# Kernel tuning notes

Measured on AMD Instinct MI355X. Metric: run time of the kernel, lower is better.

The kernel has to match this reference:

```python
import jax, jax.numpy as jnp
import numpy as np

H = 8
D_MODEL = 512
D_K = D_MODEL // H
B = 8
S = 1024


def _linear(x, W, b):
    # torch nn.Linear: y = x @ W.T + b, W: [out, in]
    return jnp.einsum('bsd,ed->bse', x, W) + b


def _to_heads(x):
    # [B,S,D] -> [B,H,S,d_k]
    return x.reshape(B, S, H, D_K).transpose(0, 2, 1, 3)


def setup_inputs() -> dict:
    key = jax.random.key(0)
    ks = jax.random.split(key, 20)
    inp = {
        'input_rgb': jax.random.normal(ks[0], (B, S, D_MODEL), jnp.float32),
        'input_flow': jax.random.normal(ks[1], (B, S, D_MODEL), jnp.float32),
    }
    names = ['Wq1', 'Wk1', 'Wv1', 'Wq2', 'Wk2', 'Wv2', 'Wo1', 'Wo2']
    for i, n in enumerate(names):
        inp[n] = jax.random.normal(ks[2 + i], (D_MODEL, D_MODEL), jnp.float32) * 0.02
        inp['b' + n[1:]] = jax.random.normal(ks[10 + i], (D_MODEL,), jnp.float32) * 0.02
    return inp


def reference(input_rgb, input_flow, Wq1, bq1, Wk1, bk1, Wv1, bv1,
              Wq2, bq2, Wk2, bk2, Wv2, bv2, Wo1, bo1, Wo2, bo2):
    scale = 1.0 / jnp.sqrt(jnp.asarray(D_K, input_rgb.dtype))

    q_r = _to_heads(_linear(input_rgb, Wq1, bq1))
    k_r = _to_heads(_linear(input_rgb, Wk1, bk1))
    v_r = _to_heads(_linear(input_rgb, Wv1, bv1))
    q_f = _to_heads(_linear(input_flow, Wq2, bq2))
    k_f = _to_heads(_linear(input_flow, Wk2, bk2))
    v_f = _to_heads(_linear(input_flow, Wv2, bv2))

    # two full [B,H,S,S] softmax attention maps
    attn_rgb = jax.nn.softmax(jnp.einsum('bhqd,bhkd->bhqk', q_r, k_r) * scale, axis=-1)
    attn_flow = jax.nn.softmax(jnp.einsum('bhqd,bhkd->bhqk', q_f, k_f) * scale, axis=-1)
    # elementwise max merge (breaks flash-attention fusion)
    attn = jnp.maximum(attn_rgb, attn_flow)

    # Attention2: out = attn @ value (dropout is identity in eval mode)
    out_rgb = jnp.einsum('bhqk,bhkd->bhqd', attn, v_r)
    out_flow = jnp.einsum('bhqk,bhkd->bhqd', attn, v_f)

    out_rgb = out_rgb.transpose(0, 2, 1, 3).reshape(B, S, D_MODEL)
    out_flow = out_flow.transpose(0, 2, 1, 3).reshape(B, S, D_MODEL)
    return (_linear(out_rgb, Wo1, bo1), _linear(out_flow, Wo2, bo2))
```

## Files before the change

### kernel.cpp

```cpp
#include <hip/hip_runtime.h>
#include <hip/hip_bf16.h>


typedef unsigned short u16;
typedef __attribute__((ext_vector_type(8))) short short8;
typedef __attribute__((ext_vector_type(4))) short s4pack;
typedef __attribute__((ext_vector_type(4))) float floatx4;

#define B_DIM 8
#define S_DIM 1024
#define H_DIM 8
#define DK 64
#define DMODEL 512
#define NTOK (B_DIM * S_DIM)
#define SEG ((size_t)NTOK * DMODEL)
#define WSEG ((size_t)DMODEL * DMODEL)

#define SCHED_FENCE() __builtin_amdgcn_sched_barrier(0)
#define LGKM0() asm volatile("s_waitcnt lgkmcnt(0)" ::: "memory")
#define BARRIER() __builtin_amdgcn_s_barrier()

__device__ __forceinline__ floatx4 mfma_bf16(short8 a, short8 b, floatx4 c) {
  return __builtin_amdgcn_mfma_f32_16x16x32_bf16(a, b, c, 0, 0, 0);
}

__device__ __forceinline__ u16 f32_to_bf16_rne(float f) {
  unsigned u = __float_as_uint(f);
  unsigned r = u + 0x7FFFu + ((u >> 16) & 1u);
  return (u16)(r >> 16);
}

__device__ __forceinline__ float bf16_bits_to_f32(u16 u) {
  return __uint_as_float(((unsigned)u) << 16);
}

__device__ __forceinline__ void async_cp16(const u16* g, u16* lds) {
  __builtin_amdgcn_global_load_lds(
      (__attribute__((address_space(1))) void*)(const_cast<u16*>(g)),
      (__attribute__((address_space(3))) void*)(lds), 16, 0, 0);
}

#define NT_CONV 18
#define CCHUNK 8192
struct ConvParams {
  const void* src[NT_CONV];
  u16* dst[NT_CONV];
  int n[NT_CONV];
  int coff[NT_CONV + 1];
};

__global__ __launch_bounds__(256) void convert_inputs(ConvParams p) {
  __shared__ int flag_f32;
  const int blk = blockIdx.x;
  int t = 0;
  while (t + 1 < NT_CONV && blk >= p.coff[t + 1]) ++t;
  const int lc = blk - p.coff[t];
  const int n = p.n[t];
  const int tid = threadIdx.x;

  if (tid < 64) {
    const u16* s = (const u16*)p.src[t];
    int bad = 0;
#pragma unroll
    for (int j = 0; j < 8; ++j) {
      float f = bf16_bits_to_f32(s[tid * 8 + j]);
      bad |= !(fabsf(f) < 1e4f);
    }
    bad |= __shfl_xor(bad, 1);
    bad |= __shfl_xor(bad, 2);
    bad |= __shfl_xor(bad, 4);
    bad |= __shfl_xor(bad, 8);
    bad |= __shfl_xor(bad, 16);
    bad |= __shfl_xor(bad, 32);
    if (tid == 0) flag_f32 = bad;
  }
  __syncthreads();
  const int is_f32 = flag_f32;
  const int base = lc * CCHUNK;

#pragma unroll
  for (int it = 0; it < CCHUNK / 2048; ++it) {
    const int idx = base + (it * 256 + tid) * 8;
    if (idx + 8 > n) break;
    if (!is_f32) {
      *(short8*)&p.dst[t][idx] = *(const short8*)&((const u16*)p.src[t])[idx];
    } else {
      const float* s = (const float*)p.src[t] + idx;
      short8 o;
#pragma unroll
      for (int j = 0; j < 8; ++j) o[j] = (short)f32_to_bf16_rne(s[j]);
      *(short8*)&p.dst[t][idx] = o;
    }
  }
}

__device__ __forceinline__ void gemm128_mainloop(
    const u16* __restrict__ A, const u16* __restrict__ W,
    int m0, int n0, u16* ldsA, u16* ldsB, floatx4 acc[4][4]) {
  const int tid = threadIdx.x;
  const int lane = tid & 63;
  const int wid = tid >> 6;
  const int wm = wid >> 1, wn = wid & 1;
  const int r = lane & 15, g = lane >> 4;

  const int stg_row = wid * 32 + (lane >> 2);
  const int stg_col = (lane & 3) * 8;

  const u16* ga0 = A + (size_t)(m0 + stg_row) * DMODEL + stg_col;
  const u16* ga1 = A + (size_t)(m0 + stg_row + 16) * DMODEL + stg_col;
  const u16* gb0 = W + (size_t)(n0 + stg_row) * DMODEL + stg_col;
  const u16* gb1 = W + (size_t)(n0 + stg_row + 16) * DMODEL + stg_col;
  const int lo0 = (wid * 32) * 32;
  const int lo1 = (wid * 32 + 16) * 32;

#pragma unroll
  for (int t = 0; t < 3; ++t) {
    const int nb = t * 4096;
    const int ko = t * 32;
    async_cp16(ga0 + ko, ldsA + nb + lo0);
    async_cp16(ga1 + ko, ldsA + nb + lo1);
    async_cp16(gb0 + ko, ldsB + nb + lo0);
    async_cp16(gb1 + ko, ldsB + nb + lo1);
  }

#pragma unroll
  for (int kt = 0; kt < 16; ++kt) {
    SCHED_FENCE();
    if (kt < 14)       asm volatile("s_waitcnt vmcnt(8)" ::: "memory");
    else if (kt == 14) asm volatile("s_waitcnt vmcnt(4)" ::: "memory");
    else               asm volatile("s_waitcnt vmcnt(0)" ::: "memory");
    BARRIER();
    SCHED_FENCE();

    const int cb = (kt % 3) * 4096;
    short8 a[4], b[4];
#pragma unroll
    for (int i = 0; i < 4; ++i)
      a[i] = *(const short8*)&ldsA[cb + (wm * 64 + i * 16 + r) * 32 + g * 8];
#pragma unroll
    for (int j = 0; j < 4; ++j)
      b[j] = *(const short8*)&ldsB[cb + (wn * 64 + j * 16 + r) * 32 + g * 8];
#pragma unroll
    for (int i = 0; i < 4; ++i)
#pragma unroll
      for (int j = 0; j < 4; ++j)
        acc[i][j] = mfma_bf16(a[i], b[j], acc[i][j]);

    if (kt + 3 < 16) {
      SCHED_FENCE(); BARRIER(); SCHED_FENCE();
      const int ko = (kt + 3) * 32;
      async_cp16(ga0 + ko, ldsA + cb + lo0);
      async_cp16(ga1 + ko, ldsA + cb + lo1);
      async_cp16(gb0 + ko, ldsB + cb + lo0);
      async_cp16(gb1 + ko, ldsB + cb + lo1);
    }
  }
}

struct QkvParams {
  const u16* X[2];
  const u16* W[2][3];
  const u16* Bias[2][3];
  u16* Out[2][3];
};

__global__ __launch_bounds__(256) void qkv_gemm(QkvParams p) {
  __shared__ u16 ldsA[3 * 128 * 32];
  __shared__ u16 ldsB[3 * 128 * 32];
  const int lin = blockIdx.x;
  const int wg = (lin & 7) * 192 + (lin >> 3);
  const int m0 = (wg / 24) * 128;
  const int c = wg % 24;
  const int z = c / 12;
  const int yc = c % 12;
  const int wi = yc >> 2;
  const int n0 = (yc & 3) * 128;

  floatx4 acc[4][4];
  const floatx4 z4 = {0.f, 0.f, 0.f, 0.f};
#pragma unroll
  for (int i = 0; i < 4; ++i)
#pragma unroll
    for (int j = 0; j < 4; ++j) acc[i][j] = z4;

  gemm128_mainloop(p.X[z], p.W[z][wi], m0, n0, ldsA, ldsB, acc);

  const int tid = threadIdx.x, lane = tid & 63, wid = tid >> 6;
  const int wm = wid >> 1, wn = wid & 1, r = lane & 15, g = lane >> 4;
  const u16* bias = p.Bias[z][wi];
  u16* out = p.Out[z][wi];
  const float qscale = 0.125f * 1.4426950408889634f;

#pragma unroll
  for (int j = 0; j < 4; ++j) {
    const int cc = n0 + wn * 64 + j * 16 + r;
    const float bv = bf16_bits_to_f32(bias[cc]);
    const int h = cc >> 6, d = cc & 63;
#pragma unroll
    for (int i = 0; i < 4; ++i) {
      const int row0 = m0 + wm * 64 + i * 16 + g * 4;
      const int bb = row0 >> 10, ss0 = row0 & 1023;
      if (wi == 2) {
        s4pack pk;
#pragma unroll
        for (int ii = 0; ii < 4; ++ii)
          pk[ii] = (short)f32_to_bf16_rne(acc[i][j][ii] + bv);
        *(s4pack*)&out[(((size_t)(bb * H_DIM + h)) * DK + d) * S_DIM + ss0] = pk;
      } else {
#pragma unroll
        for (int ii = 0; ii < 4; ++ii) {
          float v = acc[i][j][ii] + bv;
          if (wi == 0) v *= qscale;
          out[(((size_t)(bb * H_DIM + h)) * S_DIM + (ss0 + ii)) * DK + d] =
              f32_to_bf16_rne(v);
        }
      }
    }
  }
}

#define KVB 32
#define QB 128

struct AttnParams {
  const u16* Q[2];
  const u16* K[2];
  const u16* Vt[2];
  u16* O[2];
};

__global__ __launch_bounds__(256, 2) void attn_merged(AttnParams p) {
  __shared__ u16 Ks[2][KVB * 64];
  __shared__ u16 Vs[2][64 * KVB];

  const int tid = threadIdx.x;
  const int lane = tid & 63;
  const int wid = tid >> 6;
  const int r = lane & 15, g = lane >> 4;

  const int lin = blockIdx.x;
  const int w = (lin & 7) * 64 + (lin >> 3);
  const int bh = w >> 3;
  const int q0 = (w & 7) * QB;
  const size_t hbase = (size_t)bh * S_DIM * DK;

  const int krow = tid >> 3, kch = tid & 7;
  const int sKr = (krow & 3) | (((krow >> 3) & 1) << 2);
  const int kdst = krow * 64 + ((kch ^ sKr) * 8);
  const size_t kgsrc = (size_t)krow * DK + kch * 8;
  const int vrow = tid >> 2, vch = tid & 3;
  const int vdst = vrow * KVB + ((vch ^ ((vrow >> 2) & 3)) * 8);
  const size_t vgsrc = (size_t)vrow * S_DIM + vch * 8;

  const int srg = (r & 3) | (((r >> 2) & 1) << 2);
  const int rowAo = ((r >> 2) * 8 + (r & 3)) * 64;
  const int cA0 = (g ^ srg) * 8;
  const int cA1 = ((4 + g) ^ srg) * 8;

  short8 qf[2][2][2];
#pragma unroll
  for (int s = 0; s < 2; ++s)
#pragma unroll
    for (int mt = 0; mt < 2; ++mt)
#pragma unroll
      for (int kc = 0; kc < 2; ++kc)
        qf[s][mt][kc] = *(const short8*)
            &p.Q[s][hbase + (size_t)(q0 + wid * 32 + mt * 16 + r) * DK +
                    kc * 32 + g * 8];

  short8 kst[2], vst[2];
#pragma unroll
  for (int s = 0; s < 2; ++s)
    kst[s] = *(const short8*)&p.K[s][hbase + kgsrc];

  const floatx4 z4 = {0.f, 0.f, 0.f, 0.f};
  float sl[2][2] = {{0.f, 0.f}, {0.f, 0.f}};

  for (int kt = 0; kt < 32; ++kt) {
    if (kt) { SCHED_FENCE(); BARRIER(); SCHED_FENCE(); }
#pragma unroll
    for (int s = 0; s < 2; ++s)
      *(short8*)&Ks[s][kdst] = kst[s];
    if (kt < 31) {
      const size_t k0n = (size_t)(kt + 1) * KVB * DK;
#pragma unroll
      for (int s = 0; s < 2; ++s)
        kst[s] = *(const short8*)&p.K[s][hbase + k0n + kgsrc];
    }
    SCHED_FENCE(); LGKM0(); BARRIER(); SCHED_FENCE();

#pragma unroll
    for (int s = 0; s < 2; ++s) {
      const short8 kA0 = *(const short8*)&Ks[s][rowAo + cA0];
      const short8 kA1 = *(const short8*)&Ks[s][rowAo + cA1];
      const short8 kB0 = *(const short8*)&Ks[s][rowAo + 256 + cA0];
      const short8 kB1 = *(const short8*)&Ks[s][rowAo + 256 + cA1];
#pragma unroll
      for (int mt = 0; mt < 2; ++mt) {
        floatx4 aA = mfma_bf16(kA0, qf[s][mt][0], z4);
        aA = mfma_bf16(kA1, qf[s][mt][1], aA);
        floatx4 aB = mfma_bf16(kB0, qf[s][mt][0], z4);
        aB = mfma_bf16(kB1, qf[s][mt][1], aB);
        sl[s][mt] += __builtin_amdgcn_exp2f(aA[0]) + __builtin_amdgcn_exp2f(aA[1]) +
                     __builtin_amdgcn_exp2f(aA[2]) + __builtin_amdgcn_exp2f(aA[3]) +
                     __builtin_amdgcn_exp2f(aB[0]) + __builtin_amdgcn_exp2f(aB[1]) +
                     __builtin_amdgcn_exp2f(aB[2]) + __builtin_amdgcn_exp2f(aB[3]);
      }
    }
  }

#pragma unroll
  for (int s = 0; s < 2; ++s) {
    kst[s] = *(const short8*)&p.K[s][hbase + kgsrc];
    vst[s] = *(const short8*)&p.Vt[s][hbase + vgsrc];
  }

  float inv_[2][2];
#pragma unroll
  for (int s = 0; s < 2; ++s)
#pragma unroll
    for (int mt = 0; mt < 2; ++mt) {
      float v = sl[s][mt];
      v += __shfl_xor(v, 16);
      v += __shfl_xor(v, 32);
      inv_[s][mt] = 1.0f / v;
    }

  floatx4 o_[2][2][4];
#pragma unroll
  for (int s = 0; s < 2; ++s)
#pragma unroll
    for (int mt = 0; mt < 2; ++mt)
#pragma unroll
      for (int nt = 0; nt < 4; ++nt) o_[s][mt][nt] = z4;

  for (int kt = 0; kt < 32; ++kt) {
    SCHED_FENCE(); BARRIER(); SCHED_FENCE();
#pragma unroll
    for (int s = 0; s < 2; ++s) {
      *(short8*)&Ks[s][kdst] = kst[s];
      *(short8*)&Vs[s][vdst] = vst[s];
    }
    if (kt < 31) {
      const size_t kn = (size_t)(kt + 1) * KVB;
#pragma unroll
      for (int s = 0; s < 2; ++s) {
        kst[s] = *(const short8*)&p.K[s][hbase + kn * DK + kgsrc];
        vst[s] = *(const short8*)&p.Vt[s][hbase + vgsrc + kn];
      }
    }
    SCHED_FENCE(); LGKM0(); BARRIER(); SCHED_FENCE();

    short8 kA0[2], kA1[2], kB0[2], kB1[2];
#pragma unroll
    for (int s = 0; s < 2; ++s) {
      kA0[s] = *(const short8*)&Ks[s][rowAo + cA0];
      kA1[s] = *(const short8*)&Ks[s][rowAo + cA1];
      kB0[s] = *(const short8*)&Ks[s][rowAo + 256 + cA0];
      kB1[s] = *(const short8*)&Ks[s][rowAo + 256 + cA1];
    }

    short8 pA[2];
#pragma unroll
    for (int mt = 0; mt < 2; ++mt) {
      floatx4 arA = mfma_bf16(kA0[0], qf[0][mt][0], z4);
      arA = mfma_bf16(kA1[0], qf[0][mt][1], arA);
      floatx4 arB = mfma_bf16(kB0[0], qf[0][mt][0], z4);
      arB = mfma_bf16(kB1[0], qf[0][mt][1], arB);
      floatx4 afA = mfma_bf16(kA0[1], qf[1][mt][0], z4);
      afA = mfma_bf16(kA1[1], qf[1][mt][1], afA);
      floatx4 afB = mfma_bf16(kB0[1], qf[1][mt][0], z4);
      afB = mfma_bf16(kB1[1], qf[1][mt][1], afB);
#pragma unroll
      for (int i = 0; i < 4; ++i) {
        const float prA = __builtin_amdgcn_exp2f(arA[i]) * inv_[0][mt];
        const float pfA = __builtin_amdgcn_exp2f(afA[i]) * inv_[1][mt];
        pA[mt][i] = (short)f32_to_bf16_rne(fmaxf(prA, pfA));
        const float prB = __builtin_amdgcn_exp2f(arB[i]) * inv_[0][mt];
        const float pfB = __builtin_amdgcn_exp2f(afB[i]) * inv_[1][mt];
        pA[mt][4 + i] = (short)f32_to_bf16_rne(fmaxf(prB, pfB));
      }
    }

    short8 vB[2][4];
#pragma unroll
    for (int s = 0; s < 2; ++s)
#pragma unroll
      for (int nt = 0; nt < 4; ++nt)
        vB[s][nt] = *(const short8*)
            &Vs[s][(nt * 16 + r) * KVB + ((g ^ ((r >> 2) & 3)) * 8)];

#pragma unroll
    for (int s = 0; s < 2; ++s)
#pragma unroll
      for (int mt = 0; mt < 2; ++mt)
#pragma unroll
        for (int nt = 0; nt < 4; ++nt)
          o_[s][mt][nt] = mfma_bf16(pA[mt], vB[s][nt], o_[s][mt][nt]);
  }

  const int bb = bh >> 3, h = bh & 7;
#pragma unroll
  for (int s = 0; s < 2; ++s) {
    u16* out = p.O[s];
#pragma unroll
    for (int mt = 0; mt < 2; ++mt)
#pragma unroll
      for (int nt = 0; nt < 4; ++nt) {
        const int col = h * 64 + nt * 16 + r;
#pragma unroll
        for (int i = 0; i < 4; ++i) {
          const int row = q0 + wid * 32 + mt * 16 + g * 4 + i;
          out[((size_t)bb * S_DIM + row) * DMODEL + col] =
              f32_to_bf16_rne(o_[s][mt][nt][i]);
        }
      }
  }
}

struct OutParams {
  const u16* A[2];
  const u16* W[2];
  const u16* Bias[2];
  float* Out[2];
};

__global__ __launch_bounds__(256) void out_gemm(OutParams p) {
  __shared__ u16 ldsA[3 * 128 * 32];
  __shared__ u16 ldsB[3 * 128 * 32];
  const int lin = blockIdx.x;
  const int wg = (lin & 7) * 64 + (lin >> 3);
  const int m0 = (wg >> 3) * 128;
  const int c = wg & 7;
  const int z = c >> 2;
  const int n0 = (c & 3) * 128;

  floatx4 acc[4][4];
  const floatx4 z4 = {0.f, 0.f, 0.f, 0.f};
#pragma unroll
  for (int i = 0; i < 4; ++i)
#pragma unroll
    for (int j = 0; j < 4; ++j) acc[i][j] = z4;

  gemm128_mainloop(p.A[z], p.W[z], m0, n0, ldsA, ldsB, acc);

  const int tid = threadIdx.x, lane = tid & 63, wid = tid >> 6;
  const int wm = wid >> 1, wn = wid & 1, r = lane & 15, g = lane >> 4;
  const u16* bias = p.Bias[z];
  float* out = p.Out[z];

#pragma unroll
  for (int j = 0; j < 4; ++j) {
    const int cc = n0 + wn * 64 + j * 16 + r;
    const float bv = bf16_bits_to_f32(bias[cc]);
#pragma unroll
    for (int i = 0; i < 4; ++i) {
      const int row0 = m0 + wm * 64 + i * 16 + g * 4;
#pragma unroll
      for (int ii = 0; ii < 4; ++ii)
        out[(size_t)(row0 + ii) * DMODEL + cc] = acc[i][j][ii] + bv;
    }
  }
}

extern "C" void kernel_launch(void* const* d_in, const int* in_sizes, int n_in,
                              void* d_out, int out_size, void* d_ws, size_t ws_size,
                              hipStream_t stream) {
  (void)in_sizes; (void)n_in; (void)out_size; (void)ws_size;
  u16* ws = (u16*)d_ws;
  u16* Qr = ws + 0 * SEG;
  u16* Kr = ws + 1 * SEG;
  u16* Vr = ws + 2 * SEG;
  u16* Qf = ws + 3 * SEG;
  u16* Kf = ws + 4 * SEG;
  u16* Vf = ws + 5 * SEG;
  u16* Or = ws + 6 * SEG;
  u16* Of = ws + 7 * SEG;
  u16* cW = ws + 8 * SEG;
  u16* cB = cW + 8 * WSEG;

  ConvParams cp;
  int coff = 0;
  for (int i = 0; i < NT_CONV; ++i) {
    cp.src[i] = d_in[i];
    int n;
    if (i < 2) {
      n = (int)SEG;
      cp.dst[i] = (i == 0) ? Or : Of;
    } else {
      const int k = (i - 2) >> 1;
      const int isb = (i - 2) & 1;
      n = isb ? DMODEL : (int)WSEG;
      cp.dst[i] = isb ? (cB + k * DMODEL) : (cW + k * WSEG);
    }
    cp.n[i] = n;
    cp.coff[i] = coff;
    coff += (n + CCHUNK - 1) / CCHUNK;
  }
  cp.coff[NT_CONV] = coff;
  convert_inputs<<<dim3(coff), dim3(256), 0, stream>>>(cp);

  QkvParams qp;
  qp.X[0] = Or;
  qp.X[1] = Of;
  for (int s = 0; s < 2; ++s)
    for (int wi = 0; wi < 3; ++wi) {
      const int k = s * 3 + wi;
      qp.W[s][wi] = cW + k * WSEG;
      qp.Bias[s][wi] = cB + k * DMODEL;
    }
  qp.Out[0][0] = Qr; qp.Out[0][1] = Kr; qp.Out[0][2] = Vr;
  qp.Out[1][0] = Qf; qp.Out[1][1] = Kf; qp.Out[1][2] = Vf;
  qkv_gemm<<<dim3(1536), dim3(256), 0, stream>>>(qp);

  AttnParams ap;
  ap.Q[0] = Qr; ap.Q[1] = Qf;
  ap.K[0] = Kr; ap.K[1] = Kf;
  ap.Vt[0] = Vr; ap.Vt[1] = Vf;
  ap.O[0] = Or; ap.O[1] = Of;
  attn_merged<<<dim3(512), dim3(256), 0, stream>>>(ap);

  OutParams op;
  op.A[0] = Or; op.A[1] = Of;
  op.W[0] = cW + 6 * WSEG; op.Bias[0] = cB + 6 * DMODEL;
  op.W[1] = cW + 7 * WSEG; op.Bias[1] = cB + 7 * DMODEL;
  op.Out[0] = (float*)d_out;
  op.Out[1] = (float*)d_out + SEG;
  out_gemm<<<dim3(512), dim3(256), 0, stream>>>(op);
}
```

Before: 232.4 us.

## Double attention KV tile to 64 and swizzle GEMM LDS layout

The attention kernel now processes 64 keys per iteration instead of 32. This halves the number of loop trips and block barriers in both the softmax-sum pass and the output pass, at the cost of more staging registers and twice the LDS for K and V. The V tile gets a new XOR swizzle over 8 chunks to match the wider row. The projection GEMM main loop also XOR-swizzles its LDS column chunks on both the async copy and the fragment reads, to reduce LDS bank conflicts.

```diff
diff --git a/kernel.cpp b/kernel.cpp
--- a/kernel.cpp
+++ b/kernel.cpp
@@ -104,7 +104,7 @@
   const int r = lane & 15, g = lane >> 4;
 
   const int stg_row = wid * 32 + (lane >> 2);
-  const int stg_col = (lane & 3) * 8;
+  const int stg_col = (((lane & 3) ^ ((lane >> 3) & 3)) * 8);
 
   const u16* ga0 = A + (size_t)(m0 + stg_row) * DMODEL + stg_col;
   const u16* ga1 = A + (size_t)(m0 + stg_row + 16) * DMODEL + stg_col;
@@ -123,6 +123,8 @@
     async_cp16(gb1 + ko, ldsB + nb + lo1);
   }
 
+  const int rc = ((g ^ ((r >> 1) & 3)) * 8);
+
 #pragma unroll
   for (int kt = 0; kt < 16; ++kt) {
     SCHED_FENCE();
@@ -136,10 +138,10 @@
     short8 a[4], b[4];
 #pragma unroll
     for (int i = 0; i < 4; ++i)
-      a[i] = *(const short8*)&ldsA[cb + (wm * 64 + i * 16 + r) * 32 + g * 8];
+      a[i] = *(const short8*)&ldsA[cb + (wm * 64 + i * 16 + r) * 32 + rc];
 #pragma unroll
     for (int j = 0; j < 4; ++j)
-      b[j] = *(const short8*)&ldsB[cb + (wn * 64 + j * 16 + r) * 32 + g * 8];
+      b[j] = *(const short8*)&ldsB[cb + (wn * 64 + j * 16 + r) * 32 + rc];
 #pragma unroll
     for (int i = 0; i < 4; ++i)
 #pragma unroll
@@ -219,7 +221,7 @@
   }
 }
 
-#define KVB 32
+#define KVB 64
 #define QB 128
 
 struct AttnParams {
@@ -245,15 +247,21 @@
   const size_t hbase = (size_t)bh * S_DIM * DK;
 
   const int krow = tid >> 3, kch = tid & 7;
-  const int sKr = (krow & 3) | (((krow >> 3) & 1) << 2);
-  const int kdst = krow * 64 + ((kch ^ sKr) * 8);
-  const size_t kgsrc = (size_t)krow * DK + kch * 8;
-  const int vrow = tid >> 2, vch = tid & 3;
-  const int vdst = vrow * KVB + ((vch ^ ((vrow >> 2) & 3)) * 8);
-  const size_t vgsrc = (size_t)vrow * S_DIM + vch * 8;
+  const int sK = (krow & 3) | (((krow >> 3) & 1) << 2);
+  const int kdst0 = krow * 64 + ((kch ^ sK) * 8);
+  const int kdst1 = (krow + 32) * 64 + ((kch ^ sK) * 8);
+  const size_t kg0 = (size_t)krow * DK + kch * 8;
+  const size_t kg1 = kg0 + (size_t)32 * DK;
+
+  const int vrow = tid >> 3, vch = tid & 7;
+  const int sV = vrow & 7;
+  const int vdst0 = vrow * KVB + ((vch ^ sV) * 8);
+  const int vdst1 = (vrow + 32) * KVB + ((vch ^ sV) * 8);
+  const size_t vg0 = (size_t)vrow * S_DIM + vch * 8;
+  const size_t vg1 = vg0 + (size_t)32 * S_DIM;
 
   const int srg = (r & 3) | (((r >> 2) & 1) << 2);
-  const int rowAo = ((r >> 2) * 8 + (r & 3)) * 64;
+  const int prow = ((r >> 2) * 8 + (r & 3)) * 64;
   const int cA0 = (g ^ srg) * 8;
   const int cA1 = ((4 + g) ^ srg) * 8;
 
@@ -268,51 +276,63 @@
             &p.Q[s][hbase + (size_t)(q0 + wid * 32 + mt * 16 + r) * DK +
                     kc * 32 + g * 8];
 
-  short8 kst[2], vst[2];
-#pragma unroll
-  for (int s = 0; s < 2; ++s)
-    kst[s] = *(const short8*)&p.K[s][hbase + kgsrc];
+  short8 kst[2][2], vst[2][2];
+#pragma unroll
+  for (int s = 0; s < 2; ++s) {
+    kst[s][0] = *(const short8*)&p.K[s][hbase + kg0];
+    kst[s][1] = *(const short8*)&p.K[s][hbase + kg1];
+  }
 
   const floatx4 z4 = {0.f, 0.f, 0.f, 0.f};
   float sl[2][2] = {{0.f, 0.f}, {0.f, 0.f}};
 
-  for (int kt = 0; kt < 32; ++kt) {
+  for (int kt = 0; kt < 16; ++kt) {
     if (kt) { SCHED_FENCE(); BARRIER(); SCHED_FENCE(); }
 #pragma unroll
-    for (int s = 0; s < 2; ++s)
-      *(short8*)&Ks[s][kdst] = kst[s];
-    if (kt < 31) {
+    for (int s = 0; s < 2; ++s) {
+      *(short8*)&Ks[s][kdst0] = kst[s][0];
+      *(short8*)&Ks[s][kdst1] = kst[s][1];
+    }
+    if (kt < 15) {
       const size_t k0n = (size_t)(kt + 1) * KVB * DK;
 #pragma unroll
-      for (int s = 0; s < 2; ++s)
-        kst[s] = *(const short8*)&p.K[s][hbase + k0n + kgsrc];
+      for (int s = 0; s < 2; ++s) {
+        kst[s][0] = *(const short8*)&p.K[s][hbase + k0n + kg0];
+        kst[s][1] = *(const short8*)&p.K[s][hbase + k0n + kg1];
+      }
     }
     SCHED_FENCE(); LGKM0(); BARRIER(); SCHED_FENCE();
 
 #pragma unroll
-    for (int s = 0; s < 2; ++s) {
-      const short8 kA0 = *(const short8*)&Ks[s][rowAo + cA0];
-      const short8 kA1 = *(const short8*)&Ks[s][rowAo + cA1];
-      const short8 kB0 = *(const short8*)&Ks[s][rowAo + 256 + cA0];
-      const short8 kB1 = *(const short8*)&Ks[s][rowAo + 256 + cA1];
-#pragma unroll
-      for (int mt = 0; mt < 2; ++mt) {
-        floatx4 aA = mfma_bf16(kA0, qf[s][mt][0], z4);
-        aA = mfma_bf16(kA1, qf[s][mt][1], aA);
-        floatx4 aB = mfma_bf16(kB0, qf[s][mt][0], z4);
-        aB = mfma_bf16(kB1, qf[s][mt][1], aB);
-        sl[s][mt] += __builtin_amdgcn_exp2f(aA[0]) + __builtin_amdgcn_exp2f(aA[1]) +
-                     __builtin_amdgcn_exp2f(aA[2]) + __builtin_amdgcn_exp2f(aA[3]) +
-                     __builtin_amdgcn_exp2f(aB[0]) + __builtin_amdgcn_exp2f(aB[1]) +
-                     __builtin_amdgcn_exp2f(aB[2]) + __builtin_amdgcn_exp2f(aB[3]);
+    for (int kb = 0; kb < 2; ++kb) {
+      const int ro = kb * 2048 + prow;
+#pragma unroll
+      for (int s = 0; s < 2; ++s) {
+        const short8 kA0 = *(const short8*)&Ks[s][ro + cA0];
+        const short8 kA1 = *(const short8*)&Ks[s][ro + cA1];
+        const short8 kB0 = *(const short8*)&Ks[s][ro + 256 + cA0];
+        const short8 kB1 = *(const short8*)&Ks[s][ro + 256 + cA1];
+#pragma unroll
+        for (int mt = 0; mt < 2; ++mt) {
+          floatx4 aA = mfma_bf16(kA0, qf[s][mt][0], z4);
+          aA = mfma_bf16(kA1, qf[s][mt][1], aA);
+          floatx4 aB = mfma_bf16(kB0, qf[s][mt][0], z4);
+          aB = mfma_bf16(kB1, qf[s][mt][1], aB);
+          sl[s][mt] += __builtin_amdgcn_exp2f(aA[0]) + __builtin_amdgcn_exp2f(aA[1]) +
+                       __builtin_amdgcn_exp2f(aA[2]) + __builtin_amdgcn_exp2f(aA[3]) +
+                       __builtin_amdgcn_exp2f(aB[0]) + __builtin_amdgcn_exp2f(aB[1]) +
+                       __builtin_amdgcn_exp2f(aB[2]) + __builtin_amdgcn_exp2f(aB[3]);
+        }
       }
     }
   }
 
 #pragma unroll
   for (int s = 0; s < 2; ++s) {
-    kst[s] = *(const short8*)&p.K[s][hbase + kgsrc];
-    vst[s] = *(const short8*)&p.Vt[s][hbase + vgsrc];
+    kst[s][0] = *(const short8*)&p.K[s][hbase + kg0];
+    kst[s][1] = *(const short8*)&p.K[s][hbase + kg1];
+    vst[s][0] = *(const short8*)&p.Vt[s][hbase + vg0];
+    vst[s][1] = *(const short8*)&p.Vt[s][hbase + vg1];
   }
 
   float inv_[2][2];
@@ -334,69 +354,77 @@
 #pragma unroll
       for (int nt = 0; nt < 4; ++nt) o_[s][mt][nt] = z4;
 
-  for (int kt = 0; kt < 32; ++kt) {
+  for (int kt = 0; kt < 16; ++kt) {
     SCHED_FENCE(); BARRIER(); SCHED_FENCE();
 #pragma unroll
     for (int s = 0; s < 2; ++s) {
-      *(short8*)&Ks[s][kdst] = kst[s];
-      *(short8*)&Vs[s][vdst] = vst[s];
-    }
-    if (kt < 31) {
-      const size_t kn = (size_t)(kt + 1) * KVB;
+      *(short8*)&Ks[s][kdst0] = kst[s][0];
+      *(short8*)&Ks[s][kdst1] = kst[s][1];
+      *(short8*)&Vs[s][vdst0] = vst[s][0];
+      *(short8*)&Vs[s][vdst1] = vst[s][1];
+    }
+    if (kt < 15) {
+      const size_t knk = (size_t)(kt + 1) * KVB;
 #pragma unroll
       for (int s = 0; s < 2; ++s) {
-        kst[s] = *(const short8*)&p.K[s][hbase + kn * DK + kgsrc];
-        vst[s] = *(const short8*)&p.Vt[s][hbase + vgsrc + kn];
+        kst[s][0] = *(const short8*)&p.K[s][hbase + knk * DK + kg0];
+        kst[s][1] = *(const short8*)&p.K[s][hbase + knk * DK + kg1];
+        vst[s][0] = *(const short8*)&p.Vt[s][hbase + vg0 + knk];
+        vst[s][1] = *(const short8*)&p.Vt[s][hbase + vg1 + knk];
       }
     }
     SCHED_FENCE(); LGKM0(); BARRIER(); SCHED_FENCE();
 
-    short8 kA0[2], kA1[2], kB0[2], kB1[2];
-#pragma unroll
-    for (int s = 0; s < 2; ++s) {
-      kA0[s] = *(const short8*)&Ks[s][rowAo + cA0];
-      kA1[s] = *(const short8*)&Ks[s][rowAo + cA1];
-      kB0[s] = *(const short8*)&Ks[s][rowAo + 256 + cA0];
-      kB1[s] = *(const short8*)&Ks[s][rowAo + 256 + cA1];
-    }
-
-    short8 pA[2];
-#pragma unroll
-    for (int mt = 0; mt < 2; ++mt) {
-      floatx4 arA = mfma_bf16(kA0[0], qf[0][mt][0], z4);
-      arA = mfma_bf16(kA1[0], qf[0][mt][1], arA);
-      floatx4 arB = mfma_bf16(kB0[0], qf[0][mt][0], z4);
-      arB = mfma_bf16(kB1[0], qf[0][mt][1], arB);
-      floatx4 afA = mfma_bf16(kA0[1], qf[1][mt][0], z4);
-      afA = mfma_bf16(kA1[1], qf[1][mt][1], afA);
-      floatx4 afB = mfma_bf16(kB0[1], qf[1][mt][0], z4);
-      afB = mfma_bf16(kB1[1], qf[1][mt][1], afB);
-#pragma unroll
-      for (int i = 0; i < 4; ++i) {
-        const float prA = __builtin_amdgcn_exp2f(arA[i]) * inv_[0][mt];
-        const float pfA = __builtin_amdgcn_exp2f(afA[i]) * inv_[1][mt];
-        pA[mt][i] = (short)f32_to_bf16_rne(fmaxf(prA, pfA));
-        const float prB = __builtin_amdgcn_exp2f(arB[i]) * inv_[0][mt];
-        const float pfB = __builtin_amdgcn_exp2f(afB[i]) * inv_[1][mt];
-        pA[mt][4 + i] = (short)f32_to_bf16_rne(fmaxf(prB, pfB));
-      }
-    }
-
-    short8 vB[2][4];
-#pragma unroll
-    for (int s = 0; s < 2; ++s)
-#pragma unroll
-      for (int nt = 0; nt < 4; ++nt)
-        vB[s][nt] = *(const short8*)
-            &Vs[s][(nt * 16 + r) * KVB + ((g ^ ((r >> 2) & 3)) * 8)];
-
-#pragma unroll
-    for (int s = 0; s < 2; ++s)
-#pragma unroll
-      for (int mt = 0; mt < 2; ++mt)
+#pragma unroll
+    for (int kb = 0; kb < 2; ++kb) {
+      const int ro = kb * 2048 + prow;
+      short8 kA0[2], kA1[2], kB0[2], kB1[2];
+#pragma unroll
+      for (int s = 0; s < 2; ++s) {
+        kA0[s] = *(const short8*)&Ks[s][ro + cA0];
+        kA1[s] = *(const short8*)&Ks[s][ro + cA1];
+        kB0[s] = *(const short8*)&Ks[s][ro + 256 + cA0];
+        kB1[s] = *(const short8*)&Ks[s][ro + 256 + cA1];
+      }
+
+      short8 pA[2];
+#pragma unroll
+      for (int mt = 0; mt < 2; ++mt) {
+        floatx4 arA = mfma_bf16(kA0[0], qf[0][mt][0], z4);
+        arA = mfma_bf16(kA1[0], qf[0][mt][1], arA);
+        floatx4 arB = mfma_bf16(kB0[0], qf[0][mt][0], z4);
+        arB = mfma_bf16(kB1[0], qf[0][mt][1], arB);
+        floatx4 afA = mfma_bf16(kA0[1], qf[1][mt][0], z4);
+        afA = mfma_bf16(kA1[1], qf[1][mt][1], afA);
+        floatx4 afB = mfma_bf16(kB0[1], qf[1][mt][0], z4);
+        afB = mfma_bf16(kB1[1], qf[1][mt][1], afB);
+#pragma unroll
+        for (int i = 0; i < 4; ++i) {
+          const float prA = __builtin_amdgcn_exp2f(arA[i]) * inv_[0][mt];
+          const float pfA = __builtin_amdgcn_exp2f(afA[i]) * inv_[1][mt];
+          pA[mt][i] = (short)f32_to_bf16_rne(fmaxf(prA, pfA));
+          const float prB = __builtin_amdgcn_exp2f(arB[i]) * inv_[0][mt];
+          const float pfB = __builtin_amdgcn_exp2f(afB[i]) * inv_[1][mt];
+          pA[mt][4 + i] = (short)f32_to_bf16_rne(fmaxf(prB, pfB));
+        }
+      }
+
+      short8 vB[2][4];
+#pragma unroll
+      for (int s = 0; s < 2; ++s)
 #pragma unroll
         for (int nt = 0; nt < 4; ++nt)
-          o_[s][mt][nt] = mfma_bf16(pA[mt], vB[s][nt], o_[s][mt][nt]);
+          vB[s][nt] = *(const short8*)
+              &Vs[s][(nt * 16 + r) * KVB + (((kb * 4 + g) ^ (r & 7)) * 8)];
+
+#pragma unroll
+      for (int s = 0; s < 2; ++s)
+#pragma unroll
+        for (int mt = 0; mt < 2; ++mt)
+#pragma unroll
+          for (int nt = 0; nt < 4; ++nt)
+            o_[s][mt][nt] = mfma_bf16(pA[mt], vB[s][nt], o_[s][mt][nt]);
+    }
   }
 
   const int bb = bh >> 3, h = bh & 7;
```

After: 232.5 us. About the same (+0.1%).
